# Performance work log

Hardware: AMD Instinct MI355X
Metric: run time of the kernel (lower is better)

## Reference

```python
import jax, jax.numpy as jnp
import numpy as np

IN_DIM = 1024
HID = 1024
OUT = 64
N_SAMPLES = 16384
LR = 0.01
EPS = 1e-8


def setup_inputs() -> dict:
    key = jax.random.key(0)
    k1, k2 = jax.random.split(key)
    training_data = jax.random.normal(k1, (N_SAMPLES, IN_DIM), dtype=jnp.float32)
    training_targets = jax.random.uniform(k2, (N_SAMPLES, OUT), dtype=jnp.float32)
    # Parameters exactly as in __init__: weights filled with 0.01, biases zero.
    w1 = jnp.full((IN_DIM, HID), 0.01, dtype=jnp.float32)
    b1 = jnp.zeros((HID,), dtype=jnp.float32)
    w2 = jnp.full((HID, HID), 0.01, dtype=jnp.float32)
    b2 = jnp.zeros((HID,), dtype=jnp.float32)
    w3 = jnp.full((HID, OUT), 0.01, dtype=jnp.float32)
    b3 = jnp.zeros((OUT,), dtype=jnp.float32)
    return {"training_data": training_data, "training_targets": training_targets,
            "w1": w1, "b1": b1, "w2": w2, "b2": b2, "w3": w3, "b3": b3}


def _normalize(w, b):
    wn = jnp.maximum(jnp.sqrt(jnp.sum(w * w)), EPS)
    bn = jnp.maximum(jnp.sqrt(jnp.sum(b * b)), EPS)
    return w / wn, b / bn


def _train(training_data, training_targets, w1, b1, w2, b2, w3, b3):
    def step(carry, xs):
        w1, b1, w2, b2, w3, b3 = carry
        x, t = xs
        # forward
        a1 = jax.nn.sigmoid(x @ w1 + b1)      # [HID]
        a2 = jax.nn.sigmoid(a1 @ w2 + b2)     # [HID]
        a3 = jax.nn.sigmoid(a2 @ w3 + b3)     # [OUT]
        e = jnp.exp(-a3)                      # softmax of negated values
        net = e / jnp.sum(e)
        # manual backprop (matches C-style code exactly)
        da1 = a1 * (1.0 - a1)
        da2 = a2 * (1.0 - a2)
        da3 = a3 * (1.0 - a3)
        d3 = (t - net) * da3                  # [OUT]
        dw3 = jnp.outer(a2, d3)               # [HID, OUT]
        o2 = (w3 @ d3) * da2                  # [HID]
        dw2 = jnp.outer(a1, o2)               # [HID, HID]
        o1 = (w2 @ o2) * da1                  # [HID]
        dw1 = jnp.outer(x, o1)                # [IN_DIM, HID]
        # update
        w1 = w1 - LR * dw1; b1 = b1 - LR * o1
        w2 = w2 - LR * dw2; b2 = b2 - LR * o2
        w3 = w3 - LR * dw3; b3 = b3 - LR * d3
        # L2 normalize each weight/bias
        w1, b1 = _normalize(w1, b1)
        w2, b2 = _normalize(w2, b2)
        w3, b3 = _normalize(w3, b3)
        return (w1, b1, w2, b2, w3, b3), None

    carry0 = (w1, b1, w2, b2, w3, b3)
    (w1, b1, w2, b2, w3, b3), _ = jax.lax.scan(step, carry0, (training_data, training_targets))
    return w1, w2, w3


def reference(training_data, training_targets, w1, b1, w2, b2, w3, b3):
    return _train(training_data, training_targets, w1, b1, w2, b2, w3, b3)
```

## Files before the change

kernel.cpp:

```cpp
#include <hip/hip_runtime.h>
#include <math.h>


#define NSTEP 16384
#define INDIM 1024
#define HID   1024
#define OUTD  64
#define LR    0.01f
#define EPSN  1e-8f

#define NWG   256
#define TPB   1024
#define CW    4
#define NBANK 8
#define P3B   8
#define CSTR  32

#define OFF_ARRIVE   0
#define OFF_RELEASE  512
#define OFF_PCNT     1024
#define OFF_QCNT     2048
#define OFF_U        4096
#define OFF_O1R      (OFF_U + HID)
#define OFF_P3       (OFF_O1R + 2*NBANK*HID)
#define OFF_ACC      (OFF_P3 + 2*P3B*OUTD)
#define OFF_SDOT     (OFF_ACC + 2*16*32)
#define OFF_NORMX    (OFF_SDOT + NSTEP)


__device__ __forceinline__ float dload(const float* p){
  return __hip_atomic_load(p, __ATOMIC_RELAXED, __HIP_MEMORY_SCOPE_AGENT);
}
__device__ __forceinline__ void dstore(float* p, float v){
  __hip_atomic_store(p, v, __ATOMIC_RELAXED, __HIP_MEMORY_SCOPE_AGENT);
}
__device__ __forceinline__ int rload(const int* p){
  return __hip_atomic_load(p, __ATOMIC_RELAXED, __HIP_MEMORY_SCOPE_AGENT);
}
__device__ __forceinline__ void rstore(int* p, int v){
  __hip_atomic_store(p, v, __ATOMIC_RELAXED, __HIP_MEMORY_SCOPE_AGENT);
}
__device__ __forceinline__ void iadd(int* p){
  __hip_atomic_fetch_add(p, 1, __ATOMIC_RELAXED, __HIP_MEMORY_SCOPE_AGENT);
}
__device__ __forceinline__ float wredf(float v){
  #pragma unroll
  for (int m = 32; m; m >>= 1) v += __shfl_xor(v, m, 64);
  return v;
}
__device__ __forceinline__ float sigf(float z){ return 1.f/(1.f+__expf(-z)); }

__global__ __launch_bounds__(64) void bp_init(const float* __restrict__ x, float* wsf){
  const int t = blockIdx.x, tid = threadIdx.x;
  const float* xt = x + (size_t)t * INDIM;
  const float* xp = x + (size_t)(t > 0 ? t - 1 : 0) * INDIM;
  float sp = 0.f, nx = 0.f;
  #pragma unroll
  for (int e = 0; e < INDIM/64; e++){
    int i = tid + 64*e; float a = xt[i];
    nx += a*a; sp += a*xp[i];
  }
  sp = wredf(sp); nx = wredf(nx);
  if (tid == 0){ wsf[OFF_SDOT + t] = (t > 0) ? sp : 0.f; wsf[OFF_NORMX + t] = nx; }
  if (blockIdx.x == 0){
    int* wsi = (int*)wsf;
    for (int i = tid; i < 256; i += 64) wsi[OFF_ARRIVE + i] = 0;
    if (tid == 0) wsi[OFF_RELEASE] = 0;
    if (tid < 16){ wsi[OFF_PCNT + CSTR*tid] = 0; wsi[OFF_QCNT + CSTR*tid] = 0; }
    for (int i = tid; i < 2*NBANK*HID; i += 64) wsf[OFF_O1R + i] = 0.f;
    for (int i = tid; i < 2*P3B*OUTD;  i += 64) wsf[OFF_P3 + i]  = 0.f;
    for (int i = tid; i < 2*16*32;     i += 64) wsf[OFF_ACC + i] = 0.f;
    __syncthreads();
    if (tid == 0){
      float* acc1 = wsf + OFF_ACC + 16*32;
      acc1[0] = 1.f; acc1[1] = 1.f; acc1[2] = 1.f; acc1[5] = 1.f;
    }
  }
}

__global__ __launch_bounds__(TPB) void bp_train(
    const float* __restrict__ xdat, const float* __restrict__ tgt,
    const float* __restrict__ w1g, const float* __restrict__ b1g,
    const float* __restrict__ w2g, const float* __restrict__ b2g,
    const float* __restrict__ w3g, const float* __restrict__ b3g,
    float* __restrict__ out, float* wsf)
{
  alignas(16) __shared__ float s1r[HID*CW];
  alignas(16) __shared__ float s2[CW*HID];
  __shared__ float s3[CW*OUTD];
  alignas(16) __shared__ float a1b[2][HID];
  __shared__ float d1s[HID];
  __shared__ float b1s[HID];
  __shared__ float o1f[HID];
  __shared__ float d3b[2][OUTD];
  __shared__ float p3r[OUTD];
  __shared__ float b3s[OUTD];
  __shared__ float o2l[CW], d2l[CW], b2l[CW];
  __shared__ float a2b[2][CW];
  __shared__ float ascr[256];

  const int tid = threadIdx.x;
  const int wg  = blockIdx.x;
  int*   arrive  = (int*)wsf + OFF_ARRIVE;
  int*   release = (int*)wsf + OFF_RELEASE;
  int*   PCNT    = (int*)wsf + OFF_PCNT;
  int*   QCNT    = (int*)wsf + OFF_QCNT;
  float* U   = wsf + OFF_U;
  float* O1R = wsf + OFF_O1R;
  float* P3  = wsf + OFF_P3;
  float* AC  = wsf + OFF_ACC;
  float* SD  = wsf + OFF_SDOT;
  float* NX  = wsf + OFF_NORMX;
  const int bank  = wg & 15;
  const int obank = wg & (NBANK-1);
  const int bank3 = wg & (P3B-1);
  const int wid   = tid >> 6;

  {
    const float4 wv = *reinterpret_cast<const float4*>(&w1g[(size_t)tid*HID + wg*CW]);
    *reinterpret_cast<float4*>(&s1r[4*tid]) = wv;
  }
  for (int v = tid; v < CW*HID; v += TPB){
    int j = v & (CW-1); int i = v >> 2;
    s2[j*HID + i] = w2g[(size_t)i*HID + wg*CW + j];
  }
  if (tid < CW*OUTD){
    int i = tid >> 6; int k = tid & 63;
    s3[tid] = w3g[(size_t)(wg*CW + i)*OUTD + k];
  }
  b1s[tid] = b1g[tid]; d1s[tid] = 0.f; o1f[tid] = 0.f; a1b[1][tid] = 0.f;
  if (tid < OUTD){ b3s[tid] = b3g[tid]; d3b[1][tid] = 0.f; p3r[tid] = 0.f; }
  if (tid < CW){
    b2l[tid] = b2g[wg*CW + tid];
    o2l[tid] = 0.f; d2l[tid] = 0.f; a2b[0][tid] = 0.f; a2b[1][tid] = 0.f;
  }
  __syncthreads();

  float xr0, xr1;

  {
    float xv = xdat[tid];
    xr0 = xv; xr1 = xv;
    float4 w = *reinterpret_cast<const float4*>(&s1r[4*tid]);
    float u0_ = wredf(xv*w.x), u1_ = wredf(xv*w.y);
    float u2_ = wredf(xv*w.z), u3_ = wredf(xv*w.w);
    if ((tid & 63) == 0){
      ascr[wid*4+0]=u0_; ascr[wid*4+1]=u1_; ascr[wid*4+2]=u2_; ascr[wid*4+3]=u3_;
    }
    __syncthreads();
    if (tid < CW){
      float s = 0.f;
      for (int w2_ = 0; w2_ < 16; w2_++) s += ascr[w2_*4 + tid];
      dstore(&U[wg*CW + tid], s);
    }
  }
  {
    asm volatile("s_waitcnt vmcnt(0) lgkmcnt(0)" ::: "memory");
    __syncthreads();
    if (tid == 0) rstore(&arrive[wg], 1);
    if (wg == 0){
      if (tid < NWG){ while (rload(&arrive[tid]) < 1) __builtin_amdgcn_s_sleep(1); }
      __syncthreads();
      if (tid == 0) rstore(release, 1);
    }
    if (tid == 0){ while (rload(release) < 1) __builtin_amdgcn_s_sleep(1); }
    __syncthreads();
    asm volatile("" ::: "memory");
  }

  for (int t = 0; t <= NSTEP; t++){
    const int p = t & 1, qq = p ^ 1;
    float* a1c = a1b[p];  float* a1p = a1b[qq];
    float* a2c = a2b[p];  float* a2p = a2b[qq];
    float* d3c = d3b[p];  float* d3p = d3b[qq];

    float nxp = NX[t > 0 ? t - 1 : 0];
    float sdt = SD[t < NSTEP ? t : 0];
    float tv_pf = (t < NSTEP && tid < OUTD) ? tgt[(size_t)t*OUTD + tid] : 0.f;

    if (tid < 112){
      int s = tid >> 4, b = tid & 15;
      ascr[128 + s*16 + b] = dload(&AC[(qq*16 + b)*32 + s]);
    }
    float u0 = dload(&U[tid]);
    float r0 = 0.f;
    #pragma unroll
    for (int b = 0; b < NBANK; b++)
      r0 += dload(&O1R[(qq*NBANK + b)*HID + tid]);
    float a1p0 = a1p[tid];
    float of0 = r0 * a1p0 * (1.f - a1p0);
    o1f[tid] = of0;

    {
      float v0 = d1s[tid]*of0;
      float v1 = of0*of0;
      float Ba = b1s[tid] - LR*of0;
      float v2 = Ba*Ba;
      float v3 = a1p0*a1p0;
      v0 = wredf(v0); v1 = wredf(v1); v2 = wredf(v2); v3 = wredf(v3);
      if ((tid & 63) == 0){
        ascr[0*16+wid]=v0; ascr[1*16+wid]=v1; ascr[2*16+wid]=v2; ascr[3*16+wid]=v3;
      }
      if (tid < 64){
        float d3v = d3p[tid];
        float v4 = d3v*d3v;
        float B3 = b3s[tid] - LR*d3v; float v5 = B3*B3;
        float v6 = d3v * p3r[tid];
        v4 = wredf(v4); v5 = wredf(v5); v6 = wredf(v6);
        if (tid == 0){ ascr[244]=v4; ascr[245]=v5; ascr[246]=v6; }
      }
    }
    __syncthreads();
    if (tid < 64){
      if (tid < 4){
        float s = 0.f;
        #pragma unroll
        for (int w = 0; w < 16; w++) s += ascr[tid*16 + w];
        ascr[240 + tid] = s;
      } else if (tid >= 8 && tid < 15){
        int s_ = tid - 8;
        float s = 0.f;
        #pragma unroll
        for (int b = 0; b < 16; b++) s += ascr[128 + s_*16 + b];
        ascr[248 + s_] = s;
      }
    }
    __syncthreads();
    float dd  = ascr[240], so  = ascr[241], sb  = ascr[242], sa1 = ascr[243];
    float sd3 = ascr[244], sb3 = ascr[245], dp3 = ascr[246];
    float m1p = ascr[248], m2p = ascr[249], m3p = ascr[250], dq  = ascr[251];
    float soq = ascr[252], sB2 = ascr[253], sa2 = ascr[254];

    float n1  = fmaxf(sqrtf(fmaxf(m1p - 2.f*LR*dd  + LR*LR*nxp*so,  0.f)), EPSN);
    float nb1 = fmaxf(sqrtf(sb),  EPSN);
    float n2  = fmaxf(sqrtf(fmaxf(m2p - 2.f*LR*dq  + LR*LR*sa1*soq, 0.f)), EPSN);
    float nb2 = fmaxf(sqrtf(sB2), EPSN);
    float n3  = fmaxf(sqrtf(fmaxf(m3p - 2.f*LR*dp3 + LR*LR*sa2*sd3, 0.f)), EPSN);
    float nb3 = fmaxf(sqrtf(sb3), EPSN);
    float rn1 = 1.f/n1, rnb1 = 1.f/nb1, rn2 = 1.f/n2, rnb2 = 1.f/nb2;
    float rn3 = 1.f/n3, rnb3 = 1.f/nb3;

    {
      float B0 = (b1s[tid] - LR*of0)*rnb1; b1s[tid] = B0;
      float dn0 = (u0 - LR*of0*sdt)*rn1;   d1s[tid] = dn0;
      a1c[tid] = sigf(dn0 + B0);
    }
    __syncthreads();

    {
      int j = tid >> 8, l = tid & 255;
      float coef = LR * o2l[j];
      float4 w  = *reinterpret_cast<float4*>(&s2[j*HID + 4*l]);
      float4 ap = *reinterpret_cast<const float4*>(&a1p[4*l]);
      float4 ac = *reinterpret_cast<const float4*>(&a1c[4*l]);
      w.x = (w.x - coef*ap.x)*rn2;  w.y = (w.y - coef*ap.y)*rn2;
      w.z = (w.z - coef*ap.z)*rn2;  w.w = (w.w - coef*ap.w)*rn2;
      *reinterpret_cast<float4*>(&s2[j*HID + 4*l]) = w;
      float acc = ac.x*w.x + ac.y*w.y + ac.z*w.z + ac.w*w.w;
      float ms  = w.x*w.x + w.y*w.y + w.z*w.z + w.w*w.w;
      acc = wredf(acc); ms = wredf(ms);
      if ((tid & 63) == 0){ ascr[wid] = acc; ascr[16 + wid] = ms; }
    }
    __syncthreads();
    if (tid < CW){
      float d2 = ascr[4*tid] + ascr[4*tid+1] + ascr[4*tid+2] + ascr[4*tid+3];
      d2l[tid] = d2;
      float b2n = (b2l[tid] - LR*o2l[tid])*rnb2;
      b2l[tid] = b2n;
      a2c[tid] = sigf(d2 + b2n);
    }
    __syncthreads();
    if (tid == 64){
      float m2 = 0.f;
      #pragma unroll
      for (int w = 0; w < 16; w++) m2 += ascr[16 + w];
      unsafeAtomicAdd(&AC[(p*16 + bank)*32 + 1], m2);
      float s = 0.f;
      for (int j = 0; j < CW; j++){ float a = a2c[j]; s += a*a; }
      unsafeAtomicAdd(&AC[(p*16 + bank)*32 + 6], s);
    }

    if (tid < OUTD){
      int k = tid;
      float d3k = d3p[k];
      float contrib = 0.f, m3s = 0.f;
      #pragma unroll
      for (int i = 0; i < CW; i++){
        float w = s3[i*OUTD + k];
        w = (w - LR*a2p[i]*d3k)*rn3;
        s3[i*OUTD + k] = w;
        contrib += a2c[i]*w;
        m3s += w*w;
      }
      unsafeAtomicAdd(&P3[(p*P3B + bank3)*OUTD + k], contrib);
      m3s = wredf(m3s);
      if (k == 0) unsafeAtomicAdd(&AC[(p*16 + bank)*32 + 2], m3s);
      b3s[k] = (b3s[k] - LR*d3k)*rnb3;
    }

    if (t == NSTEP){
      __syncthreads();
      const float* xl = xdat + (size_t)(NSTEP - 1)*INDIM;
      float xv = xl[tid];
      float c0 = LR*o1f[wg*CW+0], c1 = LR*o1f[wg*CW+1];
      float c2 = LR*o1f[wg*CW+2], c3 = LR*o1f[wg*CW+3];
      float4 w = *reinterpret_cast<const float4*>(&s1r[4*tid]);
      float4 ov;
      ov.x = (w.x - c0*xv)*rn1; ov.y = (w.y - c1*xv)*rn1;
      ov.z = (w.z - c2*xv)*rn1; ov.w = (w.w - c3*xv)*rn1;
      *reinterpret_cast<float4*>(&out[(size_t)tid*HID + wg*CW]) = ov;
      float4 o2v;
      o2v.x = s2[0*HID+tid]; o2v.y = s2[1*HID+tid];
      o2v.z = s2[2*HID+tid]; o2v.w = s2[3*HID+tid];
      *reinterpret_cast<float4*>(&out[(size_t)HID*HID + (size_t)tid*HID + wg*CW]) = o2v;
      if (tid < OUTD){
        #pragma unroll
        for (int i = 0; i < CW; i++)
          out[(size_t)2*HID*HID + (size_t)(wg*CW + i)*OUTD + tid] = s3[i*OUTD + tid];
      }
      break;
    }

    if (wid == 0){
      asm volatile("s_waitcnt vmcnt(0) lgkmcnt(0)" ::: "memory");
      if (tid == 0) iadd(&PCNT[CSTR*bank]);
    }

    float u_pub = 0.f;
    {
      const float* xn_ = xdat + (size_t)(t + 1 < NSTEP ? t + 1 : NSTEP - 1)*INDIM;
      float xpv = (t & 1) ? xr0 : xr1;
      float xnv = xn_[tid];
      if (t & 1) xr0 = xnv; else xr1 = xnv;
      float c0 = LR*o1f[wg*CW+0], c1 = LR*o1f[wg*CW+1];
      float c2 = LR*o1f[wg*CW+2], c3 = LR*o1f[wg*CW+3];
      float4 w = *reinterpret_cast<float4*>(&s1r[4*tid]);
      w.x = (w.x - c0*xpv)*rn1; w.y = (w.y - c1*xpv)*rn1;
      w.z = (w.z - c2*xpv)*rn1; w.w = (w.w - c3*xpv)*rn1;
      *reinterpret_cast<float4*>(&s1r[4*tid]) = w;
      float m1s = w.x*w.x + w.y*w.y + w.z*w.z + w.w*w.w;
      float u0_ = wredf(xnv*w.x), u1_ = wredf(xnv*w.y);
      float u2_ = wredf(xnv*w.z), u3_ = wredf(xnv*w.w);
      m1s = wredf(m1s);
      if ((tid & 63) == 0){
        ascr[wid*4+0]=u0_; ascr[wid*4+1]=u1_; ascr[wid*4+2]=u2_; ascr[wid*4+3]=u3_;
        ascr[64 + wid] = m1s;
      }
      __syncthreads();
      if (tid < CW){
        float s = 0.f;
        #pragma unroll
        for (int w2_ = 0; w2_ < 16; w2_++) s += ascr[w2_*4 + tid];
        u_pub = s;
      }
      if (tid == 0){
        float m1 = 0.f;
        #pragma unroll
        for (int w2_ = 0; w2_ < 16; w2_++) m1 += ascr[64 + w2_];
        unsafeAtomicAdd(&AC[(p*16 + bank)*32 + 0], m1);
      }
    }

    {
      const int ptgt = 16*(t+1);
      if (tid < 16){
        while (rload(&PCNT[CSTR*tid]) < ptgt) __builtin_amdgcn_s_sleep(1);
      }
      __syncthreads();
      asm volatile("" ::: "memory");
    }

    if (wg < NBANK) dstore(&O1R[(qq*NBANK + wg)*HID + tid], 0.f);
    if (wg < P3B && tid < OUTD) dstore(&P3[(qq*P3B + wg)*OUTD + tid], 0.f);
    if (wg < 16  && tid < 8)    dstore(&AC[(qq*16 + wg)*32 + tid], 0.f);
    if (tid < CW) dstore(&U[wg*CW + tid], u_pub);
    float s2v0 = s2[0*HID+tid], s2v1 = s2[1*HID+tid];
    float s2v2 = s2[2*HID+tid], s2v3 = s2[3*HID+tid];

    if (tid < OUTD){
      float s = 0.f;
      #pragma unroll
      for (int b = 0; b < P3B; b++) s += dload(&P3[(p*P3B + b)*OUTD + tid]);
      p3r[tid] = s;
      float a3 = sigf(s + b3s[tid]);
      float e3 = __expf(-a3);
      float es = wredf(e3);
      float net = e3 / es;
      d3c[tid] = (tv_pf - net) * a3 * (1.f - a3);
    }
    __syncthreads();
    if (tid < CW*OUTD){
      int i = tid >> 6, k = tid & 63;
      float v = wredf(s3[i*OUTD + k] * d3c[k]);
      if (k == 0){ float a2v = a2c[i]; o2l[i] = v * a2v * (1.f - a2v); }
    }
    __syncthreads();
    if (tid == 0){
      float dd2 = 0.f, so2 = 0.f, sB2n = 0.f;
      for (int j = 0; j < CW; j++){
        float ov = o2l[j];
        dd2 += d2l[j]*ov; so2 += ov*ov;
        float B = b2l[j] - LR*ov; sB2n += B*B;
      }
      unsafeAtomicAdd(&AC[(p*16 + bank)*32 + 3], dd2);
      unsafeAtomicAdd(&AC[(p*16 + bank)*32 + 4], so2);
      unsafeAtomicAdd(&AC[(p*16 + bank)*32 + 5], sB2n);
    }
    {
      float q0 = s2v0*o2l[0] + s2v1*o2l[1] + s2v2*o2l[2] + s2v3*o2l[3];
      unsafeAtomicAdd(&O1R[(p*NBANK + obank)*HID + tid], q0);
    }
    asm volatile("s_waitcnt vmcnt(0) lgkmcnt(0)" ::: "memory");
    __syncthreads();
    if (tid == 0) iadd(&QCNT[CSTR*bank]);
    {
      const int qtgt = 16*(t+1);
      if (tid < 16){
        while (rload(&QCNT[CSTR*tid]) < qtgt) __builtin_amdgcn_s_sleep(1);
      }
      __syncthreads();
      asm volatile("" ::: "memory");
    }
  }
}

extern "C" void kernel_launch(void* const* d_in, const int* in_sizes, int n_in,
                              void* d_out, int out_size, void* d_ws, size_t ws_size,
                              hipStream_t stream){
  const float* x  = (const float*)d_in[0];
  const float* tg = (const float*)d_in[1];
  const float* w1 = (const float*)d_in[2];
  const float* b1 = (const float*)d_in[3];
  const float* w2 = (const float*)d_in[4];
  const float* b2 = (const float*)d_in[5];
  const float* w3 = (const float*)d_in[6];
  const float* b3 = (const float*)d_in[7];
  float* out = (float*)d_out;
  float* wsf = (float*)d_ws;
  hipLaunchKernelGGL(bp_init,  dim3(NSTEP), dim3(64),  0, stream, x, wsf);
  hipLaunchKernelGGL(bp_train, dim3(NWG),   dim3(TPB), 0, stream,
                     x, tg, w1, b1, w2, b2, w3, b3, out, wsf);
}
```

Before: 196.1 ms.

## Halve persistent workgroups and give each eight hidden columns instead of four

Cuts the persistent grid from 256 to 128 workgroups, each owning 8 hidden columns of w1/w2/w3 in shared memory instead of 4. The per-step loops, the reductions, the ascr scratch offsets and the barrier counter targets are all rewritten to match. The aim is to halve the number of participants in the two grid-wide barriers and the atomic traffic per step, in exchange for twice the per-workgroup compute and LDS footprint on a latency-bound serial scan.

```diff
diff --git a/kernel.cpp b/kernel.cpp
--- a/kernel.cpp
+++ b/kernel.cpp
@@ -9,9 +9,9 @@
 #define LR    0.01f
 #define EPSN  1e-8f
 
-#define NWG   256
+#define NWG   128
 #define TPB   1024
-#define CW    4
+#define CW    8
 #define NBANK 8
 #define P3B   8
 #define CSTR  32
@@ -117,11 +117,13 @@
   const int wid   = tid >> 6;
 
   {
-    const float4 wv = *reinterpret_cast<const float4*>(&w1g[(size_t)tid*HID + wg*CW]);
-    *reinterpret_cast<float4*>(&s1r[4*tid]) = wv;
+    const float4 wa = *reinterpret_cast<const float4*>(&w1g[(size_t)tid*HID + wg*CW]);
+    const float4 wb = *reinterpret_cast<const float4*>(&w1g[(size_t)tid*HID + wg*CW + 4]);
+    *reinterpret_cast<float4*>(&s1r[8*tid])     = wa;
+    *reinterpret_cast<float4*>(&s1r[8*tid + 4]) = wb;
   }
   for (int v = tid; v < CW*HID; v += TPB){
-    int j = v & (CW-1); int i = v >> 2;
+    int j = v & (CW-1); int i = v >> 3;
     s2[j*HID + i] = w2g[(size_t)i*HID + wg*CW + j];
   }
   if (tid < CW*OUTD){
@@ -141,16 +143,22 @@
   {
     float xv = xdat[tid];
     xr0 = xv; xr1 = xv;
-    float4 w = *reinterpret_cast<const float4*>(&s1r[4*tid]);
-    float u0_ = wredf(xv*w.x), u1_ = wredf(xv*w.y);
-    float u2_ = wredf(xv*w.z), u3_ = wredf(xv*w.w);
+    float4 wa = *reinterpret_cast<const float4*>(&s1r[8*tid]);
+    float4 wb = *reinterpret_cast<const float4*>(&s1r[8*tid + 4]);
+    float u_[CW];
+    u_[0] = wredf(xv*wa.x); u_[1] = wredf(xv*wa.y);
+    u_[2] = wredf(xv*wa.z); u_[3] = wredf(xv*wa.w);
+    u_[4] = wredf(xv*wb.x); u_[5] = wredf(xv*wb.y);
+    u_[6] = wredf(xv*wb.z); u_[7] = wredf(xv*wb.w);
     if ((tid & 63) == 0){
-      ascr[wid*4+0]=u0_; ascr[wid*4+1]=u1_; ascr[wid*4+2]=u2_; ascr[wid*4+3]=u3_;
+      #pragma unroll
+      for (int c = 0; c < CW; c++) ascr[96 + wid*CW + c] = u_[c];
     }
     __syncthreads();
     if (tid < CW){
       float s = 0.f;
-      for (int w2_ = 0; w2_ < 16; w2_++) s += ascr[w2_*4 + tid];
+      #pragma unroll
+      for (int w2_ = 0; w2_ < 16; w2_++) s += ascr[96 + w2_*CW + tid];
       dstore(&U[wg*CW + tid], s);
     }
   }
@@ -249,21 +257,34 @@
 
     {
       int j = tid >> 8, l = tid & 255;
-      float coef = LR * o2l[j];
-      float4 w  = *reinterpret_cast<float4*>(&s2[j*HID + 4*l]);
+      float coefA = LR * o2l[j];
+      float coefB = LR * o2l[j+4];
+      float4 wa = *reinterpret_cast<float4*>(&s2[j*HID + 4*l]);
+      float4 wb = *reinterpret_cast<float4*>(&s2[(j+4)*HID + 4*l]);
       float4 ap = *reinterpret_cast<const float4*>(&a1p[4*l]);
       float4 ac = *reinterpret_cast<const float4*>(&a1c[4*l]);
-      w.x = (w.x - coef*ap.x)*rn2;  w.y = (w.y - coef*ap.y)*rn2;
-      w.z = (w.z - coef*ap.z)*rn2;  w.w = (w.w - coef*ap.w)*rn2;
-      *reinterpret_cast<float4*>(&s2[j*HID + 4*l]) = w;
-      float acc = ac.x*w.x + ac.y*w.y + ac.z*w.z + ac.w*w.w;
-      float ms  = w.x*w.x + w.y*w.y + w.z*w.z + w.w*w.w;
-      acc = wredf(acc); ms = wredf(ms);
-      if ((tid & 63) == 0){ ascr[wid] = acc; ascr[16 + wid] = ms; }
+      wa.x = (wa.x - coefA*ap.x)*rn2;  wa.y = (wa.y - coefA*ap.y)*rn2;
+      wa.z = (wa.z - coefA*ap.z)*rn2;  wa.w = (wa.w - coefA*ap.w)*rn2;
+      wb.x = (wb.x - coefB*ap.x)*rn2;  wb.y = (wb.y - coefB*ap.y)*rn2;
+      wb.z = (wb.z - coefB*ap.z)*rn2;  wb.w = (wb.w - coefB*ap.w)*rn2;
+      *reinterpret_cast<float4*>(&s2[j*HID + 4*l])     = wa;
+      *reinterpret_cast<float4*>(&s2[(j+4)*HID + 4*l]) = wb;
+      float accA = ac.x*wa.x + ac.y*wa.y + ac.z*wa.z + ac.w*wa.w;
+      float accB = ac.x*wb.x + ac.y*wb.y + ac.z*wb.z + ac.w*wb.w;
+      float ms   = wa.x*wa.x + wa.y*wa.y + wa.z*wa.z + wa.w*wa.w
+                 + wb.x*wb.x + wb.y*wb.y + wb.z*wb.z + wb.w*wb.w;
+      accA = wredf(accA); accB = wredf(accB); ms = wredf(ms);
+      if ((tid & 63) == 0){ ascr[wid] = accA; ascr[32 + wid] = accB; ascr[16 + wid] = ms; }
     }
     __syncthreads();
     if (tid < CW){
-      float d2 = ascr[4*tid] + ascr[4*tid+1] + ascr[4*tid+2] + ascr[4*tid+3];
+      float d2;
+      if (tid < 4)
+        d2 = ascr[4*tid] + ascr[4*tid+1] + ascr[4*tid+2] + ascr[4*tid+3];
+      else {
+        int b = 32 + 4*(tid-4);
+        d2 = ascr[b] + ascr[b+1] + ascr[b+2] + ascr[b+3];
+      }
       d2l[tid] = d2;
       float b2n = (b2l[tid] - LR*o2l[tid])*rnb2;
       b2l[tid] = b2n;
@@ -304,15 +325,24 @@
       float xv = xl[tid];
       float c0 = LR*o1f[wg*CW+0], c1 = LR*o1f[wg*CW+1];
       float c2 = LR*o1f[wg*CW+2], c3 = LR*o1f[wg*CW+3];
-      float4 w = *reinterpret_cast<const float4*>(&s1r[4*tid]);
-      float4 ov;
-      ov.x = (w.x - c0*xv)*rn1; ov.y = (w.y - c1*xv)*rn1;
-      ov.z = (w.z - c2*xv)*rn1; ov.w = (w.w - c3*xv)*rn1;
-      *reinterpret_cast<float4*>(&out[(size_t)tid*HID + wg*CW]) = ov;
-      float4 o2v;
-      o2v.x = s2[0*HID+tid]; o2v.y = s2[1*HID+tid];
-      o2v.z = s2[2*HID+tid]; o2v.w = s2[3*HID+tid];
-      *reinterpret_cast<float4*>(&out[(size_t)HID*HID + (size_t)tid*HID + wg*CW]) = o2v;
+      float c4 = LR*o1f[wg*CW+4], c5 = LR*o1f[wg*CW+5];
+      float c6 = LR*o1f[wg*CW+6], c7 = LR*o1f[wg*CW+7];
+      float4 wa = *reinterpret_cast<const float4*>(&s1r[8*tid]);
+      float4 wb = *reinterpret_cast<const float4*>(&s1r[8*tid + 4]);
+      float4 ovA, ovB;
+      ovA.x = (wa.x - c0*xv)*rn1; ovA.y = (wa.y - c1*xv)*rn1;
+      ovA.z = (wa.z - c2*xv)*rn1; ovA.w = (wa.w - c3*xv)*rn1;
+      ovB.x = (wb.x - c4*xv)*rn1; ovB.y = (wb.y - c5*xv)*rn1;
+      ovB.z = (wb.z - c6*xv)*rn1; ovB.w = (wb.w - c7*xv)*rn1;
+      *reinterpret_cast<float4*>(&out[(size_t)tid*HID + wg*CW])     = ovA;
+      *reinterpret_cast<float4*>(&out[(size_t)tid*HID + wg*CW + 4]) = ovB;
+      float4 o2a, o2b;
+      o2a.x = s2[0*HID+tid]; o2a.y = s2[1*HID+tid];
+      o2a.z = s2[2*HID+tid]; o2a.w = s2[3*HID+tid];
+      o2b.x = s2[4*HID+tid]; o2b.y = s2[5*HID+tid];
+      o2b.z = s2[6*HID+tid]; o2b.w = s2[7*HID+tid];
+      *reinterpret_cast<float4*>(&out[(size_t)HID*HID + (size_t)tid*HID + wg*CW])     = o2a;
+      *reinterpret_cast<float4*>(&out[(size_t)HID*HID + (size_t)tid*HID + wg*CW + 4]) = o2b;
       if (tid < OUTD){
         #pragma unroll
         for (int i = 0; i < CW; i++)
@@ -334,35 +364,46 @@
       if (t & 1) xr0 = xnv; else xr1 = xnv;
       float c0 = LR*o1f[wg*CW+0], c1 = LR*o1f[wg*CW+1];
       float c2 = LR*o1f[wg*CW+2], c3 = LR*o1f[wg*CW+3];
-      float4 w = *reinterpret_cast<float4*>(&s1r[4*tid]);
-      w.x = (w.x - c0*xpv)*rn1; w.y = (w.y - c1*xpv)*rn1;
-      w.z = (w.z - c2*xpv)*rn1; w.w = (w.w - c3*xpv)*rn1;
-      *reinterpret_cast<float4*>(&s1r[4*tid]) = w;
-      float m1s = w.x*w.x + w.y*w.y + w.z*w.z + w.w*w.w;
-      float u0_ = wredf(xnv*w.x), u1_ = wredf(xnv*w.y);
-      float u2_ = wredf(xnv*w.z), u3_ = wredf(xnv*w.w);
+      float c4 = LR*o1f[wg*CW+4], c5 = LR*o1f[wg*CW+5];
+      float c6 = LR*o1f[wg*CW+6], c7 = LR*o1f[wg*CW+7];
+      float4 wa = *reinterpret_cast<float4*>(&s1r[8*tid]);
+      float4 wb = *reinterpret_cast<float4*>(&s1r[8*tid + 4]);
+      wa.x = (wa.x - c0*xpv)*rn1; wa.y = (wa.y - c1*xpv)*rn1;
+      wa.z = (wa.z - c2*xpv)*rn1; wa.w = (wa.w - c3*xpv)*rn1;
+      wb.x = (wb.x - c4*xpv)*rn1; wb.y = (wb.y - c5*xpv)*rn1;
+      wb.z = (wb.z - c6*xpv)*rn1; wb.w = (wb.w - c7*xpv)*rn1;
+      *reinterpret_cast<float4*>(&s1r[8*tid])     = wa;
+      *reinterpret_cast<float4*>(&s1r[8*tid + 4]) = wb;
+      float m1s = wa.x*wa.x + wa.y*wa.y + wa.z*wa.z + wa.w*wa.w
+                + wb.x*wb.x + wb.y*wb.y + wb.z*wb.z + wb.w*wb.w;
+      float u_[CW];
+      u_[0] = wredf(xnv*wa.x); u_[1] = wredf(xnv*wa.y);
+      u_[2] = wredf(xnv*wa.z); u_[3] = wredf(xnv*wa.w);
+      u_[4] = wredf(xnv*wb.x); u_[5] = wredf(xnv*wb.y);
+      u_[6] = wredf(xnv*wb.z); u_[7] = wredf(xnv*wb.w);
       m1s = wredf(m1s);
       if ((tid & 63) == 0){
-        ascr[wid*4+0]=u0_; ascr[wid*4+1]=u1_; ascr[wid*4+2]=u2_; ascr[wid*4+3]=u3_;
-        ascr[64 + wid] = m1s;
+        #pragma unroll
+        for (int c = 0; c < CW; c++) ascr[96 + wid*CW + c] = u_[c];
+        ascr[224 + wid] = m1s;
       }
       __syncthreads();
       if (tid < CW){
         float s = 0.f;
         #pragma unroll
-        for (int w2_ = 0; w2_ < 16; w2_++) s += ascr[w2_*4 + tid];
+        for (int w2_ = 0; w2_ < 16; w2_++) s += ascr[96 + w2_*CW + tid];
         u_pub = s;
       }
       if (tid == 0){
         float m1 = 0.f;
         #pragma unroll
-        for (int w2_ = 0; w2_ < 16; w2_++) m1 += ascr[64 + w2_];
+        for (int w2_ = 0; w2_ < 16; w2_++) m1 += ascr[224 + w2_];
         unsafeAtomicAdd(&AC[(p*16 + bank)*32 + 0], m1);
       }
     }
 
     {
-      const int ptgt = 16*(t+1);
+      const int ptgt = (NWG/16)*(t+1);
       if (tid < 16){
         while (rload(&PCNT[CSTR*tid]) < ptgt) __builtin_amdgcn_s_sleep(1);
       }
@@ -376,6 +417,8 @@
     if (tid < CW) dstore(&U[wg*CW + tid], u_pub);
     float s2v0 = s2[0*HID+tid], s2v1 = s2[1*HID+tid];
     float s2v2 = s2[2*HID+tid], s2v3 = s2[3*HID+tid];
+    float s2v4 = s2[4*HID+tid], s2v5 = s2[5*HID+tid];
+    float s2v6 = s2[6*HID+tid], s2v7 = s2[7*HID+tid];
 
     if (tid < OUTD){
       float s = 0.f;
@@ -407,14 +450,15 @@
       unsafeAtomicAdd(&AC[(p*16 + bank)*32 + 5], sB2n);
     }
     {
-      float q0 = s2v0*o2l[0] + s2v1*o2l[1] + s2v2*o2l[2] + s2v3*o2l[3];
+      float q0 = s2v0*o2l[0] + s2v1*o2l[1] + s2v2*o2l[2] + s2v3*o2l[3]
+               + s2v4*o2l[4] + s2v5*o2l[5] + s2v6*o2l[6] + s2v7*o2l[7];
       unsafeAtomicAdd(&O1R[(p*NBANK + obank)*HID + tid], q0);
     }
     asm volatile("s_waitcnt vmcnt(0) lgkmcnt(0)" ::: "memory");
     __syncthreads();
     if (tid == 0) iadd(&QCNT[CSTR*bank]);
     {
-      const int qtgt = 16*(t+1);
+      const int qtgt = (NWG/16)*(t+1);
       if (tid < 16){
         while (rload(&QCNT[CSTR*tid]) < qtgt) __builtin_amdgcn_s_sleep(1);
       }
```

Result: faster. 190.5 ms (-2.9%).
